# Kernel tuning notes

Measured on AMD Instinct MI355X. Metric: run time of the kernel, lower is better.

The kernel has to match this reference:

```python
import jax, jax.numpy as jnp
import numpy as np

B, S, D, R = 4, 4096, 1024, 64


def setup_inputs() -> dict:
    key = jax.random.key(0)
    k1, k2 = jax.random.split(key)
    x = jax.random.normal(k1, (B, S, D), dtype=jnp.float32)
    # nn.init.uniform_(proj, -0.05, 0.05)
    proj = jax.random.uniform(k2, (D, R), dtype=jnp.float32, minval=-0.05, maxval=0.05)
    return {"x": x, "proj": proj}


def reference(x, proj):
    # Low-rank projection: [B, S, D] @ [D, R] -> [B, S, R]
    p = jnp.matmul(x, proj)
    # Pairwise squared L2 distances via ||a||^2 + ||b||^2 - 2 a.b
    # (algebraically equal to the broadcasted (a-b)^2 sum in the original)
    sq = jnp.sum(p * p, axis=-1)                      # [B, S]
    cross = jnp.einsum("bsr,btr->bst", p, p)          # [B, S, S]
    dist = sq[:, :, None] + sq[:, None, :] - 2.0 * cross
    return jnp.maximum(dist, 0.0)
```

## Files before the change

kernel.cpp:

```cpp
#include <hip/hip_runtime.h>
#include <hip/hip_bf16.h>

#define M_TOT 16384
#define DK    1024
#define RN    64
#define SQ_S  4096

typedef __attribute__((ext_vector_type(8))) short  short8;
typedef __attribute__((ext_vector_type(4))) float  f32x4;

__device__ __forceinline__ unsigned short f2bf(float f) {
    unsigned u = __float_as_uint(f);
    return (unsigned short)((u + 0x7fffu + ((u >> 16) & 1u)) >> 16);
}
__device__ __forceinline__ float bf2f(unsigned short h) {
    return __uint_as_float((unsigned)h << 16);
}

__global__ __launch_bounds__(256) void prep_kernel(
        const float* __restrict__ proj,
        unsigned short* __restrict__ pTh,
        unsigned short* __restrict__ pTl) {
    int idx = blockIdx.x * 256 + threadIdx.x;
    int r = idx >> 10;
    int k = idx & 1023;
    float v = proj[k * RN + r];
    unsigned short hi = f2bf(v);
    pTh[idx] = hi;
    pTl[idx] = f2bf(v - bf2f(hi));
}

__global__ __launch_bounds__(256) void phase1_kernel(
        const float* __restrict__ x,
        const unsigned short* __restrict__ pTh,
        const unsigned short* __restrict__ pTl,
        unsigned short* __restrict__ p_hi,
        unsigned short* __restrict__ p_lo,
        float* __restrict__ sq) {
    const int tid  = threadIdx.x;
    const int wave = tid >> 6;
    const int lane = tid & 63;
    const int lr   = lane & 15;
    const int lg   = lane >> 4;

    const long m0   = (long)blockIdx.x * 64 + wave * 16;
    const float* xrow = x + (m0 + lr) * DK + lg * 8;

    f32x4 acc[4] = {f32x4{0,0,0,0}, f32x4{0,0,0,0}, f32x4{0,0,0,0}, f32x4{0,0,0,0}};

    for (int kc = 0; kc < DK / 32; ++kc) {
        f32x4 a0 = *(const f32x4*)(xrow + kc * 32);
        f32x4 a1 = *(const f32x4*)(xrow + kc * 32 + 4);
        short8 ah, al;
        #pragma unroll
        for (int i = 0; i < 4; ++i) {
            unsigned short h0 = f2bf(a0[i]);
            ah[i] = (short)h0;
            al[i] = (short)f2bf(a0[i] - bf2f(h0));
            unsigned short h1 = f2bf(a1[i]);
            ah[i + 4] = (short)h1;
            al[i + 4] = (short)f2bf(a1[i] - bf2f(h1));
        }
        #pragma unroll
        for (int cj = 0; cj < 4; ++cj) {
            long bo = (long)(cj * 16 + lr) * DK + kc * 32 + lg * 8;
            short8 bh = *(const short8*)(pTh + bo);
            short8 bl = *(const short8*)(pTl + bo);
            f32x4 c = acc[cj];
            c = __builtin_amdgcn_mfma_f32_16x16x32_bf16(ah, bh, c, 0, 0, 0);
            c = __builtin_amdgcn_mfma_f32_16x16x32_bf16(ah, bl, c, 0, 0, 0);
            c = __builtin_amdgcn_mfma_f32_16x16x32_bf16(al, bh, c, 0, 0, 0);
            acc[cj] = c;
        }
    }

    #pragma unroll
    for (int j = 0; j < 4; ++j) {
        const long m = m0 + lg * 4 + j;
        float ssum = 0.f;
        #pragma unroll
        for (int cj = 0; cj < 4; ++cj) {
            float v = acc[cj][j];
            unsigned short hi = f2bf(v);
            p_hi[m * RN + cj * 16 + lr] = hi;
            p_lo[m * RN + cj * 16 + lr] = f2bf(v - bf2f(hi));
            ssum += v * v;
        }
        ssum += __shfl_xor(ssum, 1);
        ssum += __shfl_xor(ssum, 2);
        ssum += __shfl_xor(ssum, 4);
        ssum += __shfl_xor(ssum, 8);
        if (lr == 0) sq[m] = ssum;
    }
}

__global__ __launch_bounds__(256) void phase2_kernel(
        const unsigned short* __restrict__ p_hi,
        const unsigned short* __restrict__ p_lo,
        const float* __restrict__ sq,
        float* __restrict__ out) {
    const int b  = blockIdx.z;
    const long s0 = (long)blockIdx.y * 128;
    const long t0 = (long)blockIdx.x * 128;
    const int tid  = threadIdx.x;
    const int wave = tid >> 6;
    const int lane = tid & 63;
    const int wr = wave >> 1, wc = wave & 1;
    const int lr = lane & 15, lg = lane >> 4;

    const unsigned short* ph  = p_hi + (long)b * SQ_S * RN;
    const unsigned short* pl  = p_lo + (long)b * SQ_S * RN;
    const float*          sqb = sq   + (long)b * SQ_S;

    f32x4 acc[4][4];
    #pragma unroll
    for (int i = 0; i < 4; ++i)
        #pragma unroll
        for (int j = 0; j < 4; ++j) acc[i][j] = f32x4{0, 0, 0, 0};

    const long arow = s0 + wr * 64 + lr;
    const long brow = t0 + wc * 64 + lr;

    #pragma unroll
    for (int kc = 0; kc < 2; ++kc) {
        short8 ah[4], al[4], bh[4], bl[4];
        #pragma unroll
        for (int i = 0; i < 4; ++i) {
            long ao = (arow + i * 16) * RN + kc * 32 + lg * 8;
            ah[i] = *(const short8*)(ph + ao);
            al[i] = *(const short8*)(pl + ao);
            long bo = (brow + i * 16) * RN + kc * 32 + lg * 8;
            bh[i] = *(const short8*)(ph + bo);
            bl[i] = *(const short8*)(pl + bo);
        }
        #pragma unroll
        for (int ai = 0; ai < 4; ++ai)
            #pragma unroll
            for (int bj = 0; bj < 4; ++bj) {
                f32x4 c = acc[ai][bj];
                c = __builtin_amdgcn_mfma_f32_16x16x32_bf16(ah[ai], bh[bj], c, 0, 0, 0);
                c = __builtin_amdgcn_mfma_f32_16x16x32_bf16(ah[ai], bl[bj], c, 0, 0, 0);
                c = __builtin_amdgcn_mfma_f32_16x16x32_bf16(al[ai], bh[bj], c, 0, 0, 0);
                acc[ai][bj] = c;
            }
    }

    float sqt[4];
    #pragma unroll
    for (int bj = 0; bj < 4; ++bj) sqt[bj] = sqb[t0 + wc * 64 + bj * 16 + lr];

    float* outb = out + (long)b * SQ_S * SQ_S;
    #pragma unroll
    for (int ai = 0; ai < 4; ++ai) {
        #pragma unroll
        for (int j = 0; j < 4; ++j) {
            long srow = s0 + wr * 64 + ai * 16 + lg * 4 + j;
            float sqs = sqb[srow];
            float* orow = outb + srow * SQ_S + t0 + wc * 64;
            #pragma unroll
            for (int bj = 0; bj < 4; ++bj) {
                float d = sqs + sqt[bj] - 2.0f * acc[ai][bj][j];
                orow[bj * 16 + lr] = fmaxf(d, 0.0f);
            }
        }
    }
}

extern "C" void kernel_launch(void* const* d_in, const int* in_sizes, int n_in,
                              void* d_out, int out_size, void* d_ws, size_t ws_size,
                              hipStream_t stream) {
    const float* x    = (const float*)d_in[0];
    const float* proj = (const float*)d_in[1];
    float* out = (float*)d_out;

    unsigned short* pTh  = (unsigned short*)d_ws;
    unsigned short* pTl  = pTh + RN * DK;
    unsigned short* p_hi = pTl + RN * DK;
    unsigned short* p_lo = p_hi + (long)M_TOT * RN;
    float*          sqp  = (float*)(p_lo + (long)M_TOT * RN);

    prep_kernel<<<(RN * DK) / 256, 256, 0, stream>>>(proj, pTh, pTl);
    phase1_kernel<<<M_TOT / 64, 256, 0, stream>>>(x, pTh, pTl, p_hi, p_lo, sqp);
    phase2_kernel<<<dim3(SQ_S / 128, SQ_S / 128, 4), 256, 0, stream>>>(p_hi, p_lo, sqp, out);
}
```

Baseline: 409.5 us.

## Split phase1 K across waves and vectorize phase2 output with nontemporal stores

```diff
diff --git a/kernel.cpp b/kernel.cpp
--- a/kernel.cpp
+++ b/kernel.cpp
@@ -43,12 +43,14 @@
     const int lr   = lane & 15;
     const int lg   = lane >> 4;
 
-    const long m0   = (long)blockIdx.x * 64 + wave * 16;
-    const float* xrow = x + (m0 + lr) * DK + lg * 8;
+    const long m0    = (long)blockIdx.x * 16;
+    const int  kbase = wave * 256;
+    const float* xrow = x + (m0 + lr) * DK + kbase + lg * 8;
 
     f32x4 acc[4] = {f32x4{0,0,0,0}, f32x4{0,0,0,0}, f32x4{0,0,0,0}, f32x4{0,0,0,0}};
 
-    for (int kc = 0; kc < DK / 32; ++kc) {
+    #pragma unroll 2
+    for (int kc = 0; kc < 8; ++kc) {
         f32x4 a0 = *(const f32x4*)(xrow + kc * 32);
         f32x4 a1 = *(const f32x4*)(xrow + kc * 32 + 4);
         short8 ah, al;
@@ -63,7 +65,7 @@
         }
         #pragma unroll
         for (int cj = 0; cj < 4; ++cj) {
-            long bo = (long)(cj * 16 + lr) * DK + kc * 32 + lg * 8;
+            long bo = (long)(cj * 16 + lr) * DK + kbase + kc * 32 + lg * 8;
             short8 bh = *(const short8*)(pTh + bo);
             short8 bl = *(const short8*)(pTl + bo);
             f32x4 c = acc[cj];
@@ -74,23 +76,35 @@
         }
     }
 
-    #pragma unroll
-    for (int j = 0; j < 4; ++j) {
-        const long m = m0 + lg * 4 + j;
-        float ssum = 0.f;
-        #pragma unroll
-        for (int cj = 0; cj < 4; ++cj) {
-            float v = acc[cj][j];
-            unsigned short hi = f2bf(v);
-            p_hi[m * RN + cj * 16 + lr] = hi;
-            p_lo[m * RN + cj * 16 + lr] = f2bf(v - bf2f(hi));
-            ssum += v * v;
-        }
-        ssum += __shfl_xor(ssum, 1);
-        ssum += __shfl_xor(ssum, 2);
-        ssum += __shfl_xor(ssum, 4);
-        ssum += __shfl_xor(ssum, 8);
-        if (lr == 0) sq[m] = ssum;
+    __shared__ float red[4][64][17];
+    #pragma unroll
+    for (int cj = 0; cj < 4; ++cj)
+        #pragma unroll
+        for (int j = 0; j < 4; ++j)
+            red[wave][lane][cj * 4 + j] = acc[cj][j];
+    __syncthreads();
+
+    if (wave == 0) {
+        #pragma unroll
+        for (int j = 0; j < 4; ++j) {
+            const long m = m0 + lg * 4 + j;
+            float ssum = 0.f;
+            #pragma unroll
+            for (int cj = 0; cj < 4; ++cj) {
+                const int sl = cj * 4 + j;
+                float v = red[0][lane][sl] + red[1][lane][sl]
+                        + red[2][lane][sl] + red[3][lane][sl];
+                unsigned short hi = f2bf(v);
+                p_hi[m * RN + cj * 16 + lr] = hi;
+                p_lo[m * RN + cj * 16 + lr] = f2bf(v - bf2f(hi));
+                ssum += v * v;
+            }
+            ssum += __shfl_xor(ssum, 1);
+            ssum += __shfl_xor(ssum, 2);
+            ssum += __shfl_xor(ssum, 4);
+            ssum += __shfl_xor(ssum, 8);
+            if (lr == 0) sq[m] = ssum;
+        }
     }
 }
 
@@ -105,7 +119,7 @@
     const int tid  = threadIdx.x;
     const int wave = tid >> 6;
     const int lane = tid & 63;
-    const int wr = wave >> 1, wc = wave & 1;
+    const int ws = wave >> 1, wt = wave & 1;
     const int lr = lane & 15, lg = lane >> 4;
 
     const unsigned short* ph  = p_hi + (long)b * SQ_S * RN;
@@ -118,50 +132,54 @@
         #pragma unroll
         for (int j = 0; j < 4; ++j) acc[i][j] = f32x4{0, 0, 0, 0};
 
-    const long arow = s0 + wr * 64 + lr;
-    const long brow = t0 + wc * 64 + lr;
+    const long trow = t0 + wt * 64 + lr;
+    const long srow = s0 + ws * 64 + lr;
 
     #pragma unroll
     for (int kc = 0; kc < 2; ++kc) {
-        short8 ah[4], al[4], bh[4], bl[4];
+        short8 th_[4], tl_[4], sh_[4], sl_[4];
         #pragma unroll
         for (int i = 0; i < 4; ++i) {
-            long ao = (arow + i * 16) * RN + kc * 32 + lg * 8;
-            ah[i] = *(const short8*)(ph + ao);
-            al[i] = *(const short8*)(pl + ao);
-            long bo = (brow + i * 16) * RN + kc * 32 + lg * 8;
-            bh[i] = *(const short8*)(ph + bo);
-            bl[i] = *(const short8*)(pl + bo);
+            long ao = (trow + i * 16) * RN + kc * 32 + lg * 8;
+            th_[i] = *(const short8*)(ph + ao);
+            tl_[i] = *(const short8*)(pl + ao);
+            long bo = (srow + i * 16) * RN + kc * 32 + lg * 8;
+            sh_[i] = *(const short8*)(ph + bo);
+            sl_[i] = *(const short8*)(pl + bo);
         }
         #pragma unroll
         for (int ai = 0; ai < 4; ++ai)
             #pragma unroll
             for (int bj = 0; bj < 4; ++bj) {
                 f32x4 c = acc[ai][bj];
-                c = __builtin_amdgcn_mfma_f32_16x16x32_bf16(ah[ai], bh[bj], c, 0, 0, 0);
-                c = __builtin_amdgcn_mfma_f32_16x16x32_bf16(ah[ai], bl[bj], c, 0, 0, 0);
-                c = __builtin_amdgcn_mfma_f32_16x16x32_bf16(al[ai], bh[bj], c, 0, 0, 0);
+                c = __builtin_amdgcn_mfma_f32_16x16x32_bf16(th_[ai], sh_[bj], c, 0, 0, 0);
+                c = __builtin_amdgcn_mfma_f32_16x16x32_bf16(th_[ai], sl_[bj], c, 0, 0, 0);
+                c = __builtin_amdgcn_mfma_f32_16x16x32_bf16(tl_[ai], sh_[bj], c, 0, 0, 0);
                 acc[ai][bj] = c;
             }
     }
 
-    float sqt[4];
-    #pragma unroll
-    for (int bj = 0; bj < 4; ++bj) sqt[bj] = sqb[t0 + wc * 64 + bj * 16 + lr];
+    f32x4 sqt[4];
+    #pragma unroll
+    for (int ai = 0; ai < 4; ++ai)
+        sqt[ai] = *(const f32x4*)(sqb + t0 + wt * 64 + ai * 16 + lg * 4);
+    float sqs[4];
+    #pragma unroll
+    for (int bj = 0; bj < 4; ++bj)
+        sqs[bj] = sqb[s0 + ws * 64 + bj * 16 + lr];
 
     float* outb = out + (long)b * SQ_S * SQ_S;
     #pragma unroll
-    for (int ai = 0; ai < 4; ++ai) {
-        #pragma unroll
-        for (int j = 0; j < 4; ++j) {
-            long srow = s0 + wr * 64 + ai * 16 + lg * 4 + j;
-            float sqs = sqb[srow];
-            float* orow = outb + srow * SQ_S + t0 + wc * 64;
+    for (int bj = 0; bj < 4; ++bj) {
+        const long s = s0 + ws * 64 + bj * 16 + lr;
+        float* orow = outb + s * SQ_S + t0 + wt * 64;
+        #pragma unroll
+        for (int ai = 0; ai < 4; ++ai) {
+            f32x4 v;
             #pragma unroll
-            for (int bj = 0; bj < 4; ++bj) {
-                float d = sqs + sqt[bj] - 2.0f * acc[ai][bj][j];
-                orow[bj * 16 + lr] = fmaxf(d, 0.0f);
-            }
+            for (int j = 0; j < 4; ++j)
+                v[j] = fmaxf(sqs[bj] + sqt[ai][j] - 2.0f * acc[ai][bj][j], 0.0f);
+            __builtin_nontemporal_store(v, (f32x4*)(orow + ai * 16 + lg * 4));
         }
     }
 }
@@ -180,6 +198,6 @@
     float*          sqp  = (float*)(p_lo + (long)M_TOT * RN);
 
     prep_kernel<<<(RN * DK) / 256, 256, 0, stream>>>(proj, pTh, pTl);
-    phase1_kernel<<<M_TOT / 64, 256, 0, stream>>>(x, pTh, pTl, p_hi, p_lo, sqp);
+    phase1_kernel<<<M_TOT / 16, 256, 0, stream>>>(x, pTh, pTl, p_hi, p_lo, sqp);
     phase2_kernel<<<dim3(SQ_S / 128, SQ_S / 128, 4), 256, 0, stream>>>(p_hi, p_lo, sqp, out);
 }
```

After: 374.2 us. -8.6%, faster.
